# Optimization experiments

Measured on AMD Instinct MI355X. Metric: run time of the kernel, lower is better.

The kernel has to match this reference:

```python
import jax, jax.numpy as jnp
import numpy as np


def setup_inputs() -> dict:
    key = jax.random.key(0)
    k1, k2 = jax.random.split(key)
    z = jax.random.normal(k1, (16, 1024, 512), dtype=jnp.float32)
    codebook = jax.random.normal(k2, (2048, 64), dtype=jnp.float32)
    return {"z": z, "codebook": codebook}


def reference(z, codebook):
    """VQQuantizer.forward: group latent, euclidean nearest-codebook quantize,
    straight-through estimator, commit loss = mse(stop_grad(z_q), z).
    Returns (codes, indices, commit_loss) matching dict values
    {'codes','indices','commit_loss'} ('z' and 'state' are z_grouped / codes).
    """
    D = codebook.shape[1]            # codebook_dim
    shp = z.shape                    # [B, T, latent]
    zg = z.reshape(shp[:-1] + (-1, D))   # [B, T, G, D]
    zf = zg.reshape(-1, D)               # [N, D], N = B*T*G
    # squared euclidean distances: ||z||^2 - 2 z.c + ||c||^2  -> [N, K]
    dist = (
        jnp.sum(zf * zf, axis=1, keepdims=True)
        - 2.0 * (zf @ codebook.T)
        + jnp.sum(codebook * codebook, axis=1)
    )
    idx = jnp.argmin(dist, axis=-1)      # [N]
    zq = codebook[idx].reshape(zg.shape)  # [B, T, G, D]
    commit_loss = jnp.mean((jax.lax.stop_gradient(zq) - zg) ** 2)
    # straight-through
    zq_st = zg + jax.lax.stop_gradient(zq - zg)
    codes = zq_st.reshape(shp)            # [B, T, latent]
    indices = idx.reshape(zg.shape[:-1])  # [B, T, G]
    return codes, indices, commit_loss
```

## Files before the change

### kernel.cpp

```cpp
#include <hip/hip_runtime.h>

typedef short s16x8 __attribute__((ext_vector_type(8)));
typedef float f32x4 __attribute__((ext_vector_type(4)));

#define CODES_ELEMS 8388608
#define N_ROWS      131072
#define IDX_OFF     CODES_ELEMS
#define LOSS_OFF    (CODES_ELEMS + N_ROWS)

#define WS_LOSS 0
#define WS_CNT  4
#define WS_CC   64
#define WS_CBS  8448
#define WS_LIST 532736
#define MARGIN_T 0.0625f

__device__ __forceinline__ float bf2f(unsigned short h) { return __uint_as_float(((unsigned)h) << 16); }
__device__ __forceinline__ unsigned short f2bf(float f) {
  unsigned u = __float_as_uint(f);
  u += 0x7fffu + ((u >> 16) & 1u);
  return (unsigned short)(u >> 16);
}
__device__ __forceinline__ void gl_lds16(const void* g, void* l) {
  __builtin_amdgcn_global_load_lds(
      (__attribute__((address_space(1))) void*)(g),
      (__attribute__((address_space(3))) void*)(l), 16, 0, 0);
}

__global__ __launch_bounds__(256) void vq_prep(const float* __restrict__ cb,
                                               float* __restrict__ cc,
                                               unsigned short* __restrict__ cbs,
                                               float* __restrict__ loss,
                                               int* __restrict__ cnt) {
  int t = threadIdx.x;
  if (blockIdx.x == 0 && t == 0) { loss[0] = 0.f; cnt[0] = 0; }
  int e = blockIdx.x * 256 + t;
  int k = e >> 7, K = e & 127;
  int s = K >> 5, rem = K & 31, q = rem >> 3, j = rem & 7;
  int d = (s < 2) ? K : (K - 64);
  float c = cb[k * 64 + d];
  unsigned short c1 = f2bf(c);
  unsigned short val = (s < 2) ? c1 : f2bf(c - bf2f(c1));
  int chunk = k >> 7, ct = (k >> 4) & 7, n = k & 15;
  cbs[(((chunk * 4 + s) * 8 + ct) * 64 + (q * 16 + n)) * 8 + j] = val;
  float sq = c * c;
  #pragma unroll
  for (int m = 1; m < 64; m <<= 1) sq += __shfl_xor(sq, m, 64);
  if ((t & 63) == 0) cc[k] = sq;
}

__global__ __launch_bounds__(256) void VQQuantizer_30064771072206_kernel(
    const float* __restrict__ zf, const unsigned short* __restrict__ cbs,
    const float* __restrict__ cc, int* __restrict__ cnt, int* __restrict__ list,
    float* __restrict__ out)
{
  __shared__ __align__(16) unsigned short bt[2][16384];
  __shared__ __align__(16) float cc_l[2048];
  const int t = threadIdx.x, w = t >> 6, l = t & 63;
  const int col = l & 15, q = l >> 4;
  const int R0 = blockIdx.x * 256;
  const float4* zf4 = (const float4*)zf;

  #pragma unroll
  for (int i = 0; i < 8; ++i) {
    int unit = i * 4 + w;
    gl_lds16(cbs + (size_t)(unit * 64 + l) * 8, &bt[0][unit * 512]);
  }
  #pragma unroll
  for (int i = 0; i < 2; ++i) {
    int idx = i * 256 + t;
    ((float4*)cc_l)[idx] = ((const float4*)cc)[idx];
  }

  s16x8 az1[4][2], az2[4][2];
  float zzr[4][4];
  #pragma unroll
  for (int tile = 0; tile < 4; ++tile) {
    int row = R0 + tile * 64 + 16 * w + col;
    const float4* zr = zf4 + (size_t)row * 16;
    float zzp = 0.f;
    #pragma unroll
    for (int s = 0; s < 2; ++s) {
      float4 u0 = zr[s * 8 + q * 2];
      float4 u1 = zr[s * 8 + q * 2 + 1];
      zzp += u0.x*u0.x + u0.y*u0.y + u0.z*u0.z + u0.w*u0.w;
      zzp += u1.x*u1.x + u1.y*u1.y + u1.z*u1.z + u1.w*u1.w;
      float m2[8] = {-2.f*u0.x, -2.f*u0.y, -2.f*u0.z, -2.f*u0.w,
                     -2.f*u1.x, -2.f*u1.y, -2.f*u1.z, -2.f*u1.w};
      #pragma unroll
      for (int j = 0; j < 8; ++j) {
        unsigned short h1 = f2bf(m2[j]);
        unsigned short h2 = f2bf(m2[j] - bf2f(h1));
        az1[tile][s][j] = (short)h1;
        az2[tile][s][j] = (short)h2;
      }
    }
    zzp += __shfl_xor(zzp, 16, 64);
    zzp += __shfl_xor(zzp, 32, 64);
    #pragma unroll
    for (int r = 0; r < 4; ++r)
      zzr[tile][r] = __shfl(zzp, q * 4 + r, 64);
  }

  unsigned p1[4][4], p2[4][4];
  #pragma unroll
  for (int tile = 0; tile < 4; ++tile)
    #pragma unroll
    for (int r = 0; r < 4; ++r) { p1[tile][r] = 0xFFFFFFFFu; p2[tile][r] = 0xFFFFFFFFu; }

  __syncthreads();

  int cur = 0;
  for (int chunk = 0; chunk < 16; ++chunk) {
    if (chunk + 1 < 16) {
      const unsigned short* src = cbs + (size_t)(chunk + 1) * 16384;
      unsigned short* dst = &bt[cur ^ 1][0];
      #pragma unroll
      for (int i = 0; i < 8; ++i) {
        int unit = i * 4 + w;
        gl_lds16(src + (size_t)(unit * 64 + l) * 8, dst + unit * 512);
      }
    }
    const unsigned short* bb = &bt[cur][l * 8];
    const float* ccc = &cc_l[chunk * 128 + col];
    #pragma unroll
    for (int ct = 0; ct < 8; ++ct) {
      float nh = ccc[ct * 16];
      const unsigned short* base = bb + ct * 512;
      s16x8 b0 = *(const s16x8*)(base);
      s16x8 b1 = *(const s16x8*)(base + 4096);
      s16x8 b2 = *(const s16x8*)(base + 8192);
      s16x8 b3 = *(const s16x8*)(base + 12288);
      unsigned pid = (unsigned)(chunk * 8 + ct);
      #pragma unroll
      for (int tile = 0; tile < 4; ++tile) {
        f32x4 acc;
        acc[0] = nh + zzr[tile][0];
        acc[1] = nh + zzr[tile][1];
        acc[2] = nh + zzr[tile][2];
        acc[3] = nh + zzr[tile][3];
        acc = __builtin_amdgcn_mfma_f32_16x16x32_bf16(az1[tile][0], b0, acc, 0, 0, 0);
        acc = __builtin_amdgcn_mfma_f32_16x16x32_bf16(az1[tile][1], b1, acc, 0, 0, 0);
        acc = __builtin_amdgcn_mfma_f32_16x16x32_bf16(az1[tile][0], b2, acc, 0, 0, 0);
        acc = __builtin_amdgcn_mfma_f32_16x16x32_bf16(az1[tile][1], b3, acc, 0, 0, 0);
        acc = __builtin_amdgcn_mfma_f32_16x16x32_bf16(az2[tile][0], b0, acc, 0, 0, 0);
        acc = __builtin_amdgcn_mfma_f32_16x16x32_bf16(az2[tile][1], b1, acc, 0, 0, 0);
        #pragma unroll
        for (int r = 0; r < 4; ++r) {
          unsigned pd = (__float_as_uint(acc[r]) & 0xFFFFFF80u) | pid;
          unsigned mx = p1[tile][r] > pd ? p1[tile][r] : pd;
          p2[tile][r] = p2[tile][r] < mx ? p2[tile][r] : mx;
          p1[tile][r] = p1[tile][r] < pd ? p1[tile][r] : pd;
        }
      }
    }
    __syncthreads();
    cur ^= 1;
  }

  #pragma unroll
  for (int tile = 0; tile < 4; ++tile) {
    #pragma unroll
    for (int r = 0; r < 4; ++r) {
      float a   = __uint_as_float(p1[tile][r] & 0xFFFFFF80u);
      int   ia  = (int)(p1[tile][r] & 127u) * 16 + col;
      float b2v = __uint_as_float(p2[tile][r] & 0xFFFFFF80u);
      #pragma unroll
      for (int m = 1; m < 16; m <<= 1) {
        float oa = __shfl_xor(a, m, 64);
        int   oi = __shfl_xor(ia, m, 64);
        float ob = __shfl_xor(b2v, m, 64);
        float hi = fmaxf(a, oa);
        b2v = fminf(fminf(b2v, ob), hi);
        bool take = (oa < a) || (oa == a && oi < ia);
        a = take ? oa : a; ia = take ? oi : ia;
      }
      if (col == 0) {
        int row = R0 + tile * 64 + 16 * w + q * 4 + r;
        out[IDX_OFF + row] = (float)ia;
        if (b2v - a < MARGIN_T) {
          int p = atomicAdd(cnt, 1);
          list[p] = row;
        }
      }
    }
  }
}

__global__ __launch_bounds__(256) void vq_rescore(
    const float* __restrict__ zf, const float* __restrict__ cb,
    const float* __restrict__ cc, const int* __restrict__ cnt,
    const int* __restrict__ list, float* __restrict__ out)
{
  __shared__ __align__(16) float zl[8][68];
  __shared__ float zz_l[8];
  __shared__ int   rows_s[8];
  __shared__ float rv[4][8];
  __shared__ int   ri[4][8];
  const int t = threadIdx.x, w = t >> 6, l = t & 63;
  const int count = cnt[0];
  const float4* cb4 = (const float4*)cb;

  for (int itb = blockIdx.x; itb * 8 < count; itb += 1024) {
    if (itb != (int)blockIdx.x) __syncthreads();
    if (t < 8) {
      int ii = itb * 8 + t;
      rows_s[t] = list[ii < count ? ii : count - 1];
    }
    __syncthreads();
    if (t < 128) {
      int r = t >> 4, dq = t & 15;
      *(float4*)&zl[r][dq * 4] = ((const float4*)zf)[(size_t)rows_s[r] * 16 + dq];
    }
    __syncthreads();
    if (t < 8) {
      float s = 0.f;
      for (int d = 0; d < 64; ++d) { float v = zl[t][d]; s += v * v; }
      zz_l[t] = s;
    }
    __syncthreads();

    float bv[8]; int bi[8];
    #pragma unroll
    for (int r = 0; r < 8; ++r) { bv[r] = 3.402823466e38f; bi[r] = 0; }
    #pragma unroll 1
    for (int o = 0; o < 8; ++o) {
      int c = o * 256 + t;
      const float4* cr = cb4 + (size_t)c * 16;
      float a[8];
      #pragma unroll
      for (int r = 0; r < 8; ++r) a[r] = 0.f;
      #pragma unroll
      for (int dq = 0; dq < 16; ++dq) {
        float4 cv = cr[dq];
        #pragma unroll
        for (int r = 0; r < 8; ++r) {
          float4 z4 = *(const float4*)&zl[r][dq * 4];
          a[r] += z4.x * cv.x;
          a[r] += z4.y * cv.y;
          a[r] += z4.z * cv.z;
          a[r] += z4.w * cv.w;
        }
      }
      float ccv = cc[c];
      #pragma unroll
      for (int r = 0; r < 8; ++r) {
        float t0 = zz_l[r] - 2.0f * a[r];
        float dist = t0 + ccv;
        if (dist < bv[r]) { bv[r] = dist; bi[r] = c; }
      }
    }
    #pragma unroll
    for (int r = 0; r < 8; ++r) {
      float v = bv[r]; int idx = bi[r];
      #pragma unroll
      for (int m = 1; m < 64; m <<= 1) {
        float ov = __shfl_xor(v, m, 64); int oi = __shfl_xor(idx, m, 64);
        if (ov < v || (ov == v && oi < idx)) { v = ov; idx = oi; }
      }
      if (l == 0) { rv[w][r] = v; ri[w][r] = idx; }
    }
    __syncthreads();
    if (t < 8) {
      float fv = rv[0][t]; int fi = ri[0][t];
      #pragma unroll
      for (int k = 1; k < 4; ++k) {
        if (rv[k][t] < fv || (rv[k][t] == fv && ri[k][t] < fi)) { fv = rv[k][t]; fi = ri[k][t]; }
      }
      out[IDX_OFF + rows_s[t]] = (float)fi;
    }
  }
}

__global__ __launch_bounds__(256) void vq_epilogue(
    const float* __restrict__ zf, const float* __restrict__ cb,
    float* __restrict__ loss, float* __restrict__ out)
{
  __shared__ int idxb[64];
  __shared__ float wsum[4];
  int t = threadIdx.x;
  int R0 = blockIdx.x * 64;
  if (t < 64) idxb[t] = (int)out[IDX_OFF + R0 + t];
  __syncthreads();
  const float4* zf4 = (const float4*)zf;
  const float4* cb4 = (const float4*)cb;
  float4* out4 = (float4*)out;
  float lsum = 0.f;
  #pragma unroll
  for (int i = 0; i < 4; ++i) {
    int f = i * 256 + t;
    int row = f >> 4, dq = f & 15;
    int k = idxb[row];
    float4 qv = cb4[(size_t)k * 16 + dq];
    float4 zv = zf4[(size_t)(R0 + row) * 16 + dq];
    float dx = qv.x - zv.x, dy = qv.y - zv.y, dz = qv.z - zv.z, dw = qv.w - zv.w;
    float4 st; st.x = zv.x + dx; st.y = zv.y + dy; st.z = zv.z + dz; st.w = zv.w + dw;
    out4[(size_t)(R0 + row) * 16 + dq] = st;
    lsum += dx * dx; lsum += dy * dy; lsum += dz * dz; lsum += dw * dw;
  }
  #pragma unroll
  for (int m = 1; m < 64; m <<= 1) lsum += __shfl_xor(lsum, m, 64);
  if ((t & 63) == 0) wsum[t >> 6] = lsum;
  __syncthreads();
  if (t == 0) atomicAdd(loss, wsum[0] + wsum[1] + wsum[2] + wsum[3]);
}

__global__ void vq_finalize(const float* __restrict__ loss, float* __restrict__ out) {
  out[LOSS_OFF] = loss[0] * (1.f / 8388608.f);
}

extern "C" void kernel_launch(void* const* d_in, const int* in_sizes, int n_in,
                              void* d_out, int out_size, void* d_ws, size_t ws_size,
                              hipStream_t stream) {
  const float* z  = (const float*)d_in[0];
  const float* cb = (const float*)d_in[1];
  float* out = (float*)d_out;
  float* loss = (float*)((char*)d_ws + WS_LOSS);
  int*   cnt  = (int*)((char*)d_ws + WS_CNT);
  float* cc   = (float*)((char*)d_ws + WS_CC);
  unsigned short* cbs = (unsigned short*)((char*)d_ws + WS_CBS);
  int*   list = (int*)((char*)d_ws + WS_LIST);

  vq_prep<<<1024, 256, 0, stream>>>(cb, cc, cbs, loss, cnt);
  VQQuantizer_30064771072206_kernel<<<512, 256, 0, stream>>>(z, cbs, cc, cnt, list, out);
  vq_rescore<<<1024, 256, 0, stream>>>(z, cb, cc, cnt, list, out);
  vq_epilogue<<<2048, 256, 0, stream>>>(z, cb, loss, out);
  vq_finalize<<<1, 1, 0, stream>>>(loss, out);
}
```

Measured before the change: 282.6 us.

## Fuse rescore and epilogue into main VQ kernel and switch to 32x32 MFMA

Folds the ambiguous-row exact rescore and the codes/loss epilogue into the main distance kernel, using LDS for indices and the flagged-row list instead of global memory and atomics. Switches the distance GEMM to 32x32x16 bf16 MFMA with a matching codebook layout, and drops the per-row ||z||^2 term in favour of a constant positive offset. This removes two kernel launches and a global round trip of indices, at the cost of serial per-block rescoring and different precision in the packed distance keys.

Measured after the change: 577.1 us. 2.04x slower.

```diff
diff --git a/kernel.cpp b/kernel.cpp
--- a/kernel.cpp
+++ b/kernel.cpp
@@ -1,7 +1,7 @@
 #include <hip/hip_runtime.h>
 
 typedef short s16x8 __attribute__((ext_vector_type(8)));
-typedef float f32x4 __attribute__((ext_vector_type(4)));
+typedef float f32x16 __attribute__((ext_vector_type(16)));
 
 #define CODES_ELEMS 8388608
 #define N_ROWS      131072
@@ -9,11 +9,10 @@
 #define LOSS_OFF    (CODES_ELEMS + N_ROWS)
 
 #define WS_LOSS 0
-#define WS_CNT  4
 #define WS_CC   64
 #define WS_CBS  8448
-#define WS_LIST 532736
 #define MARGIN_T 0.0625f
+#define DIST_OFF 512.0f
 
 __device__ __forceinline__ float bf2f(unsigned short h) { return __uint_as_float(((unsigned)h) << 16); }
 __device__ __forceinline__ unsigned short f2bf(float f) {
@@ -30,83 +29,84 @@
 __global__ __launch_bounds__(256) void vq_prep(const float* __restrict__ cb,
                                                float* __restrict__ cc,
                                                unsigned short* __restrict__ cbs,
-                                               float* __restrict__ loss,
-                                               int* __restrict__ cnt) {
+                                               float* __restrict__ loss) {
   int t = threadIdx.x;
-  if (blockIdx.x == 0 && t == 0) { loss[0] = 0.f; cnt[0] = 0; }
+  if (blockIdx.x == 0 && t == 0) loss[0] = 0.f;
   int e = blockIdx.x * 256 + t;
   int k = e >> 7, K = e & 127;
-  int s = K >> 5, rem = K & 31, q = rem >> 3, j = rem & 7;
-  int d = (s < 2) ? K : (K - 64);
+  int limb = K >> 6, d = K & 63;
   float c = cb[k * 64 + d];
   unsigned short c1 = f2bf(c);
-  unsigned short val = (s < 2) ? c1 : f2bf(c - bf2f(c1));
-  int chunk = k >> 7, ct = (k >> 4) & 7, n = k & 15;
-  cbs[(((chunk * 4 + s) * 8 + ct) * 64 + (q * 16 + n)) * 8 + j] = val;
+  unsigned short val = limb ? f2bf(c - bf2f(c1)) : c1;
+  int group = k >> 5, n = k & 31;
+  int f = limb * 4 + (d >> 4);
+  int lane = ((d >> 3) & 1) * 32 + n;
+  int j = d & 7;
+  cbs[(((size_t)group * 8 + f) * 64 + lane) * 8 + j] = val;
   float sq = c * c;
   #pragma unroll
   for (int m = 1; m < 64; m <<= 1) sq += __shfl_xor(sq, m, 64);
   if ((t & 63) == 0) cc[k] = sq;
 }
 
-__global__ __launch_bounds__(256) void VQQuantizer_30064771072206_kernel(
-    const float* __restrict__ zf, const unsigned short* __restrict__ cbs,
-    const float* __restrict__ cc, int* __restrict__ cnt, int* __restrict__ list,
-    float* __restrict__ out)
+__global__ __launch_bounds__(256, 2) void VQQuantizer_30064771072206_kernel(
+    const float* __restrict__ zf, const float* __restrict__ cb,
+    const unsigned short* __restrict__ cbs, const float* __restrict__ cc,
+    float* __restrict__ loss, float* __restrict__ out)
 {
   __shared__ __align__(16) unsigned short bt[2][16384];
   __shared__ __align__(16) float cc_l[2048];
+  int*   idx_l  = (int*)&bt[0][0];
+  int*   flg    = (int*)((char*)&bt[0][0] + 1024);
+  int*   nf     = (int*)((char*)&bt[0][0] + 2048);
+  float (*zl)[68] = (float(*)[68])((char*)&bt[0][0] + 2064);
+  float* zz_l   = (float*)((char*)&bt[0][0] + 4240);
+  int*   rows_s = (int*)((char*)&bt[0][0] + 4272);
+  float (*rv)[8] = (float(*)[8])((char*)&bt[0][0] + 4304);
+  int   (*ri)[8] = (int(*)[8])((char*)&bt[0][0] + 4432);
+  float* wsum   = (float*)((char*)&bt[0][0] + 4560);
+
   const int t = threadIdx.x, w = t >> 6, l = t & 63;
-  const int col = l & 15, q = l >> 4;
+  const int col = l & 31, hi = l >> 5;
   const int R0 = blockIdx.x * 256;
   const float4* zf4 = (const float4*)zf;
+  const float4* cb4 = (const float4*)cb;
 
   #pragma unroll
   for (int i = 0; i < 8; ++i) {
-    int unit = i * 4 + w;
-    gl_lds16(cbs + (size_t)(unit * 64 + l) * 8, &bt[0][unit * 512]);
-  }
-  #pragma unroll
-  for (int i = 0; i < 2; ++i) {
-    int idx = i * 256 + t;
-    ((float4*)cc_l)[idx] = ((const float4*)cc)[idx];
-  }
-
-  s16x8 az1[4][2], az2[4][2];
-  float zzr[4][4];
-  #pragma unroll
-  for (int tile = 0; tile < 4; ++tile) {
-    int row = R0 + tile * 64 + 16 * w + col;
+    int s0 = i * 256 + w * 64;
+    gl_lds16(cbs + (size_t)(s0 + l) * 8, &bt[0][(size_t)s0 * 8]);
+  }
+  #pragma unroll
+  for (int i = 0; i < 2; ++i)
+    ((float4*)cc_l)[i * 256 + t] = ((const float4*)cc)[i * 256 + t];
+
+  s16x8 az1[2][4], az2[2][4];
+  #pragma unroll
+  for (int tile = 0; tile < 2; ++tile) {
+    int row = R0 + w * 64 + tile * 32 + col;
     const float4* zr = zf4 + (size_t)row * 16;
-    float zzp = 0.f;
-    #pragma unroll
-    for (int s = 0; s < 2; ++s) {
-      float4 u0 = zr[s * 8 + q * 2];
-      float4 u1 = zr[s * 8 + q * 2 + 1];
-      zzp += u0.x*u0.x + u0.y*u0.y + u0.z*u0.z + u0.w*u0.w;
-      zzp += u1.x*u1.x + u1.y*u1.y + u1.z*u1.z + u1.w*u1.w;
+    #pragma unroll
+    for (int f = 0; f < 4; ++f) {
+      float4 u0 = zr[f * 4 + hi * 2];
+      float4 u1 = zr[f * 4 + hi * 2 + 1];
       float m2[8] = {-2.f*u0.x, -2.f*u0.y, -2.f*u0.z, -2.f*u0.w,
                      -2.f*u1.x, -2.f*u1.y, -2.f*u1.z, -2.f*u1.w};
       #pragma unroll
       for (int j = 0; j < 8; ++j) {
         unsigned short h1 = f2bf(m2[j]);
         unsigned short h2 = f2bf(m2[j] - bf2f(h1));
-        az1[tile][s][j] = (short)h1;
-        az2[tile][s][j] = (short)h2;
-      }
-    }
-    zzp += __shfl_xor(zzp, 16, 64);
-    zzp += __shfl_xor(zzp, 32, 64);
-    #pragma unroll
-    for (int r = 0; r < 4; ++r)
-      zzr[tile][r] = __shfl(zzp, q * 4 + r, 64);
-  }
-
-  unsigned p1[4][4], p2[4][4];
-  #pragma unroll
-  for (int tile = 0; tile < 4; ++tile)
-    #pragma unroll
-    for (int r = 0; r < 4; ++r) { p1[tile][r] = 0xFFFFFFFFu; p2[tile][r] = 0xFFFFFFFFu; }
+        az1[tile][f][j] = (short)h1;
+        az2[tile][f][j] = (short)h2;
+      }
+    }
+  }
+
+  unsigned p1[2][16], p2[2][16];
+  #pragma unroll
+  for (int tile = 0; tile < 2; ++tile)
+    #pragma unroll
+    for (int r = 0; r < 16; ++r) { p1[tile][r] = 0xFFFFFFFFu; p2[tile][r] = 0xFFFFFFFFu; }
 
   __syncthreads();
 
@@ -117,36 +117,43 @@
       unsigned short* dst = &bt[cur ^ 1][0];
       #pragma unroll
       for (int i = 0; i < 8; ++i) {
-        int unit = i * 4 + w;
-        gl_lds16(src + (size_t)(unit * 64 + l) * 8, dst + unit * 512);
-      }
-    }
-    const unsigned short* bb = &bt[cur][l * 8];
-    const float* ccc = &cc_l[chunk * 128 + col];
-    #pragma unroll
-    for (int ct = 0; ct < 8; ++ct) {
-      float nh = ccc[ct * 16];
-      const unsigned short* base = bb + ct * 512;
-      s16x8 b0 = *(const s16x8*)(base);
-      s16x8 b1 = *(const s16x8*)(base + 4096);
-      s16x8 b2 = *(const s16x8*)(base + 8192);
-      s16x8 b3 = *(const s16x8*)(base + 12288);
-      unsigned pid = (unsigned)(chunk * 8 + ct);
-      #pragma unroll
-      for (int tile = 0; tile < 4; ++tile) {
-        f32x4 acc;
-        acc[0] = nh + zzr[tile][0];
-        acc[1] = nh + zzr[tile][1];
-        acc[2] = nh + zzr[tile][2];
-        acc[3] = nh + zzr[tile][3];
-        acc = __builtin_amdgcn_mfma_f32_16x16x32_bf16(az1[tile][0], b0, acc, 0, 0, 0);
-        acc = __builtin_amdgcn_mfma_f32_16x16x32_bf16(az1[tile][1], b1, acc, 0, 0, 0);
-        acc = __builtin_amdgcn_mfma_f32_16x16x32_bf16(az1[tile][0], b2, acc, 0, 0, 0);
-        acc = __builtin_amdgcn_mfma_f32_16x16x32_bf16(az1[tile][1], b3, acc, 0, 0, 0);
-        acc = __builtin_amdgcn_mfma_f32_16x16x32_bf16(az2[tile][0], b0, acc, 0, 0, 0);
-        acc = __builtin_amdgcn_mfma_f32_16x16x32_bf16(az2[tile][1], b1, acc, 0, 0, 0);
+        int s0 = i * 256 + w * 64;
+        gl_lds16(src + (size_t)(s0 + l) * 8, dst + (size_t)s0 * 8);
+      }
+    }
+    #pragma unroll
+    for (int g = 0; g < 4; ++g) {
+      int group = chunk * 4 + g;
+      float nh = DIST_OFF + cc_l[group * 32 + col];
+      const unsigned short* base = &bt[cur][((size_t)g * 8 * 64 + l) * 8];
+      s16x8 bc0 = *(const s16x8*)(base + 0 * 512);
+      s16x8 bc1 = *(const s16x8*)(base + 1 * 512);
+      s16x8 bc2 = *(const s16x8*)(base + 2 * 512);
+      s16x8 bc3 = *(const s16x8*)(base + 3 * 512);
+      s16x8 bc4 = *(const s16x8*)(base + 4 * 512);
+      s16x8 bc5 = *(const s16x8*)(base + 5 * 512);
+      s16x8 bc6 = *(const s16x8*)(base + 6 * 512);
+      s16x8 bc7 = *(const s16x8*)(base + 7 * 512);
+      unsigned pid = (unsigned)group;
+      #pragma unroll
+      for (int tile = 0; tile < 2; ++tile) {
+        f32x16 acc;
         #pragma unroll
-        for (int r = 0; r < 4; ++r) {
+        for (int r = 0; r < 16; ++r) acc[r] = nh;
+        acc = __builtin_amdgcn_mfma_f32_32x32x16_bf16(az1[tile][0], bc0, acc, 0, 0, 0);
+        acc = __builtin_amdgcn_mfma_f32_32x32x16_bf16(az1[tile][1], bc1, acc, 0, 0, 0);
+        acc = __builtin_amdgcn_mfma_f32_32x32x16_bf16(az1[tile][2], bc2, acc, 0, 0, 0);
+        acc = __builtin_amdgcn_mfma_f32_32x32x16_bf16(az1[tile][3], bc3, acc, 0, 0, 0);
+        acc = __builtin_amdgcn_mfma_f32_32x32x16_bf16(az1[tile][0], bc4, acc, 0, 0, 0);
+        acc = __builtin_amdgcn_mfma_f32_32x32x16_bf16(az1[tile][1], bc5, acc, 0, 0, 0);
+        acc = __builtin_amdgcn_mfma_f32_32x32x16_bf16(az1[tile][2], bc6, acc, 0, 0, 0);
+        acc = __builtin_amdgcn_mfma_f32_32x32x16_bf16(az1[tile][3], bc7, acc, 0, 0, 0);
+        acc = __builtin_amdgcn_mfma_f32_32x32x16_bf16(az2[tile][0], bc0, acc, 0, 0, 0);
+        acc = __builtin_amdgcn_mfma_f32_32x32x16_bf16(az2[tile][1], bc1, acc, 0, 0, 0);
+        acc = __builtin_amdgcn_mfma_f32_32x32x16_bf16(az2[tile][2], bc2, acc, 0, 0, 0);
+        acc = __builtin_amdgcn_mfma_f32_32x32x16_bf16(az2[tile][3], bc3, acc, 0, 0, 0);
+        #pragma unroll
+        for (int r = 0; r < 16; ++r) {
           unsigned pd = (__float_as_uint(acc[r]) & 0xFFFFFF80u) | pid;
           unsigned mx = p1[tile][r] > pd ? p1[tile][r] : pd;
           p2[tile][r] = p2[tile][r] < mx ? p2[tile][r] : mx;
@@ -158,59 +165,48 @@
     cur ^= 1;
   }
 
-  #pragma unroll
-  for (int tile = 0; tile < 4; ++tile) {
-    #pragma unroll
-    for (int r = 0; r < 4; ++r) {
+  if (t == 0) *nf = 0;
+  __syncthreads();
+  #pragma unroll
+  for (int tile = 0; tile < 2; ++tile) {
+    #pragma unroll
+    for (int r = 0; r < 16; ++r) {
       float a   = __uint_as_float(p1[tile][r] & 0xFFFFFF80u);
-      int   ia  = (int)(p1[tile][r] & 127u) * 16 + col;
+      int   ia  = (int)(p1[tile][r] & 127u) * 32 + col;
       float b2v = __uint_as_float(p2[tile][r] & 0xFFFFFF80u);
       #pragma unroll
-      for (int m = 1; m < 16; m <<= 1) {
+      for (int m = 1; m < 32; m <<= 1) {
         float oa = __shfl_xor(a, m, 64);
         int   oi = __shfl_xor(ia, m, 64);
         float ob = __shfl_xor(b2v, m, 64);
-        float hi = fmaxf(a, oa);
-        b2v = fminf(fminf(b2v, ob), hi);
+        float hv = fmaxf(a, oa);
+        b2v = fminf(fminf(b2v, ob), hv);
         bool take = (oa < a) || (oa == a && oi < ia);
         a = take ? oa : a; ia = take ? oi : ia;
       }
       if (col == 0) {
-        int row = R0 + tile * 64 + 16 * w + q * 4 + r;
-        out[IDX_OFF + row] = (float)ia;
+        int rl = w * 64 + tile * 32 + 4 * hi + (r & 3) + 8 * (r >> 2);
+        idx_l[rl] = ia;
         if (b2v - a < MARGIN_T) {
-          int p = atomicAdd(cnt, 1);
-          list[p] = row;
+          int p = atomicAdd(nf, 1);
+          flg[p] = rl;
         }
       }
     }
   }
-}
-
-__global__ __launch_bounds__(256) void vq_rescore(
-    const float* __restrict__ zf, const float* __restrict__ cb,
-    const float* __restrict__ cc, const int* __restrict__ cnt,
-    const int* __restrict__ list, float* __restrict__ out)
-{
-  __shared__ __align__(16) float zl[8][68];
-  __shared__ float zz_l[8];
-  __shared__ int   rows_s[8];
-  __shared__ float rv[4][8];
-  __shared__ int   ri[4][8];
-  const int t = threadIdx.x, w = t >> 6, l = t & 63;
-  const int count = cnt[0];
-  const float4* cb4 = (const float4*)cb;
-
-  for (int itb = blockIdx.x; itb * 8 < count; itb += 1024) {
-    if (itb != (int)blockIdx.x) __syncthreads();
+  __syncthreads();
+
+  int count = *nf;
+  for (int itb = 0; itb * 8 < count; ++itb) {
+    if (itb) __syncthreads();
     if (t < 8) {
       int ii = itb * 8 + t;
-      rows_s[t] = list[ii < count ? ii : count - 1];
+      rows_s[t] = flg[ii < count ? ii : count - 1];
     }
     __syncthreads();
     if (t < 128) {
       int r = t >> 4, dq = t & 15;
-      *(float4*)&zl[r][dq * 4] = ((const float4*)zf)[(size_t)rows_s[r] * 16 + dq];
+      *(float4*)&zl[r][dq * 4] = zf4[(size_t)(R0 + rows_s[r]) * 16 + dq];
     }
     __syncthreads();
     if (t < 8) {
@@ -242,7 +238,7 @@
           a[r] += z4.w * cv.w;
         }
       }
-      float ccv = cc[c];
+      float ccv = cc_l[c];
       #pragma unroll
       for (int r = 0; r < 8; ++r) {
         float t0 = zz_l[r] - 2.0f * a[r];
@@ -267,30 +263,18 @@
       for (int k = 1; k < 4; ++k) {
         if (rv[k][t] < fv || (rv[k][t] == fv && ri[k][t] < fi)) { fv = rv[k][t]; fi = ri[k][t]; }
       }
-      out[IDX_OFF + rows_s[t]] = (float)fi;
-    }
-  }
-}
-
-__global__ __launch_bounds__(256) void vq_epilogue(
-    const float* __restrict__ zf, const float* __restrict__ cb,
-    float* __restrict__ loss, float* __restrict__ out)
-{
-  __shared__ int idxb[64];
-  __shared__ float wsum[4];
-  int t = threadIdx.x;
-  int R0 = blockIdx.x * 64;
-  if (t < 64) idxb[t] = (int)out[IDX_OFF + R0 + t];
-  __syncthreads();
-  const float4* zf4 = (const float4*)zf;
-  const float4* cb4 = (const float4*)cb;
+      idx_l[rows_s[t]] = fi;
+    }
+  }
+  __syncthreads();
+
   float4* out4 = (float4*)out;
   float lsum = 0.f;
   #pragma unroll
-  for (int i = 0; i < 4; ++i) {
+  for (int i = 0; i < 16; ++i) {
     int f = i * 256 + t;
     int row = f >> 4, dq = f & 15;
-    int k = idxb[row];
+    int k = idx_l[row];
     float4 qv = cb4[(size_t)k * 16 + dq];
     float4 zv = zf4[(size_t)(R0 + row) * 16 + dq];
     float dx = qv.x - zv.x, dy = qv.y - zv.y, dz = qv.z - zv.z, dw = qv.w - zv.w;
@@ -298,9 +282,10 @@
     out4[(size_t)(R0 + row) * 16 + dq] = st;
     lsum += dx * dx; lsum += dy * dy; lsum += dz * dz; lsum += dw * dw;
   }
+  out[IDX_OFF + R0 + t] = (float)idx_l[t];
   #pragma unroll
   for (int m = 1; m < 64; m <<= 1) lsum += __shfl_xor(lsum, m, 64);
-  if ((t & 63) == 0) wsum[t >> 6] = lsum;
+  if (l == 0) wsum[w] = lsum;
   __syncthreads();
   if (t == 0) atomicAdd(loss, wsum[0] + wsum[1] + wsum[2] + wsum[3]);
 }
@@ -316,14 +301,10 @@
   const float* cb = (const float*)d_in[1];
   float* out = (float*)d_out;
   float* loss = (float*)((char*)d_ws + WS_LOSS);
-  int*   cnt  = (int*)((char*)d_ws + WS_CNT);
   float* cc   = (float*)((char*)d_ws + WS_CC);
   unsigned short* cbs = (unsigned short*)((char*)d_ws + WS_CBS);
-  int*   list = (int*)((char*)d_ws + WS_LIST);
-
-  vq_prep<<<1024, 256, 0, stream>>>(cb, cc, cbs, loss, cnt);
-  VQQuantizer_30064771072206_kernel<<<512, 256, 0, stream>>>(z, cbs, cc, cnt, list, out);
-  vq_rescore<<<1024, 256, 0, stream>>>(z, cb, cc, cnt, list, out);
-  vq_epilogue<<<2048, 256, 0, stream>>>(z, cb, loss, out);
+
+  vq_prep<<<1024, 256, 0, stream>>>(cb, cc, cbs, loss);
+  VQQuantizer_30064771072206_kernel<<<512, 256, 0, stream>>>(z, cb, cbs, cc, loss, out);
   vq_finalize<<<1, 1, 0, stream>>>(loss, out);
 }
```
